# Kernel optimization log

Hardware: AMD Instinct MI355X
Metric: run time of the kernel (lower is better)

Reference implementation:

```python
import jax, jax.numpy as jnp
import numpy as np

#   per angular channel l: out_l = (1/sqrt(2l+1)) * sum_m x_nu[n,m,q] * x_1[n,m,p]
#   stacked over l with zero padding in the m axis (pad beyond 2l+1 is zero,
#   so the m-sum is unaffected), features flattened as full (q, p) outer product.

L = 4       # l = 0..3
N = 50000   # atomic environments (samples)
M = 7       # 2*l_max + 1
F_NU = 32   # features of density_nu per l
F_1 = 16    # features of density_1 per l


def setup_inputs() -> dict:
    key = jax.random.key(0)
    k1, k2 = jax.random.split(key)
    x_nu = jax.random.normal(k1, (L, N, M, F_NU), dtype=jnp.float32)
    x_1 = jax.random.normal(k2, (L, N, M, F_1), dtype=jnp.float32)
    ls = jnp.arange(L)
    # mask m-components beyond 2l+1 for each l  -> [L, M]
    mmask = (jnp.arange(M)[None, :] < (2 * ls + 1)[:, None]).astype(jnp.float32)
    x_nu = x_nu * mmask[:, None, :, None]
    x_1 = x_1 * mmask[:, None, :, None]
    return {"x_nu": x_nu, "x_1": x_1}


def reference(x_nu, x_1):
    # x_nu: [L, N, M, F_nu], x_1: [L, N, M, F_1]
    l_dim, n, _, f_nu = x_nu.shape
    f_1 = x_1.shape[-1]
    cg = 1.0 / jnp.sqrt(2.0 * jnp.arange(l_dim, dtype=jnp.float32) + 1.0)  # [L]
    # full (q_nu, q_1) outer product with sum over m, per l
    out = jnp.einsum('lnmq,lnmp->nlqp', x_nu, x_1)  # [N, L, F_nu, F_1]
    out = out * cg[None, :, None, None]
    return out.reshape(n, l_dim * f_nu * f_1)  # [N, L*F_nu*F_1]
```

## Files before the change

### kernel.cpp

```cpp
#include <hip/hip_runtime.h>


constexpr int L_DIM  = 4;
constexpr int M_DIM  = 7;
constexpr int FNU    = 32;
constexpr int F1     = 16;
constexpr int XNU_W  = L_DIM * M_DIM * FNU;
constexpr int X1_W   = L_DIM * M_DIM * F1;
constexpr int SAMP_W = XNU_W + X1_W;
constexpr int OUT_W  = L_DIM * FNU * F1;
constexpr int SPB    = 4;
constexpr int NV4    = SPB * SAMP_W / 4;
constexpr int NCHUNK = NV4 / 64;

typedef float f32x4 __attribute__((ext_vector_type(4)));

__global__ __launch_bounds__(256) void ps_kernel(
    const float* __restrict__ x_nu,
    const float* __restrict__ x_1,
    float* __restrict__ out,
    int N)
{
    __shared__ float lds[SPB * SAMP_W];
    const int t    = threadIdx.x;
    const int n0   = blockIdx.x * SPB;
    const int lane = t & 63;
    const int wid  = t >> 6;

    const float4* __restrict__ xnu4 = reinterpret_cast<const float4*>(x_nu);
    const float4* __restrict__ x14  = reinterpret_cast<const float4*>(x_1);
    float4* lds4 = reinterpret_cast<float4*>(lds);

    #pragma unroll
    for (int j = 0; j < 6; ++j) {
        const int c = wid + 4 * j;
        if (c < NCHUNK) {
            const int i = c * 64 + lane;
            int s = i / 336;
            int r = i - s * 336;
            int n = n0 + s;
            if (n >= N) n = N - 1;
            const float4* src;
            if (r < 224) {
                int l = r / 56, off = r - l * 56;
                src = &xnu4[(size_t)(l * N + n) * 56 + off];
            } else {
                int r2 = r - 224;
                int l = r2 / 28, off = r2 - l * 28;
                src = &x14[(size_t)(l * N + n) * 28 + off];
            }
            __builtin_amdgcn_global_load_lds(
                (const __attribute__((address_space(1))) void*)src,
                (__attribute__((address_space(3))) void*)&lds4[i],
                16, 0, 0);
        }
    }
    __syncthreads();

    const int u7 = t & 127;
    const int l  = u7 >> 5;
    const int u  = u7 & 31;
    const int pb = (u & 3) * 4;
    const int q2 = u >> 2;
    const float scale = rsqrtf(2.0f * (float)l + 1.0f);

    #pragma unroll
    for (int ss = 0; ss < 2; ++ss) {
        const int s = (t >> 7) + 2 * ss;
        const int n = n0 + s;
        if (n < N) {
            const float* xnu_s = lds + s * SAMP_W + l * (M_DIM * FNU);
            const float* x1_s  = lds + s * SAMP_W + XNU_W + l * (M_DIM * F1);

            float acc[4][4];
            #pragma unroll
            for (int k = 0; k < 4; ++k)
                #pragma unroll
                for (int j = 0; j < 4; ++j) acc[k][j] = 0.0f;

            #pragma unroll
            for (int m = 0; m < M_DIM; ++m) {
                float4 b = *reinterpret_cast<const float4*>(&x1_s[m * F1 + pb]);
                float a[4];
                #pragma unroll
                for (int k = 0; k < 4; ++k) a[k] = xnu_s[m * FNU + q2 + 8 * k];
                #pragma unroll
                for (int k = 0; k < 4; ++k) {
                    acc[k][0] += a[k] * b.x;
                    acc[k][1] += a[k] * b.y;
                    acc[k][2] += a[k] * b.z;
                    acc[k][3] += a[k] * b.w;
                }
            }

            float* outp = out + (size_t)n * OUT_W + l * (FNU * F1);
            #pragma unroll
            for (int k = 0; k < 4; ++k) {
                int q = q2 + 8 * k;
                f32x4 v = { acc[k][0] * scale, acc[k][1] * scale,
                            acc[k][2] * scale, acc[k][3] * scale };
                __builtin_nontemporal_store(v, reinterpret_cast<f32x4*>(&outp[q * F1 + pb]));
            }
        }
    }
}

extern "C" void kernel_launch(void* const* d_in, const int* in_sizes, int n_in,
                              void* d_out, int out_size, void* d_ws, size_t ws_size,
                              hipStream_t stream) {
    const float* x_nu = (const float*)d_in[0];
    const float* x_1  = (const float*)d_in[1];
    float* out = (float*)d_out;
    const int N = in_sizes[0] / XNU_W;
    const int blocks = (N + SPB - 1) / SPB;
    ps_kernel<<<blocks, 256, 0, stream>>>(x_nu, x_1, out, N);
}
```

Measured before the change: 580.8 us.

## Use persistent grid with double-buffered async LDS staging of sample groups

Replaces the one-block-per-group launch with a fixed grid of 512 persistent blocks. Each block loops over sample groups and prefetches the next group into a second LDS buffer with global_load_lds while computing the current one, using per-wave vmcnt waits and raw s_barrier. Output stores are switched from nontemporal to regular stores. The fixed grid may leave CUs underoccupied, and the hand-tuned vmcnt counts are fragile if the compiler issues a different number of loads.

```diff
diff --git a/kernel.cpp b/kernel.cpp
--- a/kernel.cpp
+++ b/kernel.cpp
@@ -10,10 +10,10 @@
 constexpr int SAMP_W = XNU_W + X1_W;
 constexpr int OUT_W  = L_DIM * FNU * F1;
 constexpr int SPB    = 4;
-constexpr int NV4    = SPB * SAMP_W / 4;
+constexpr int GRP_W  = SPB * SAMP_W;
+constexpr int NV4    = GRP_W / 4;
 constexpr int NCHUNK = NV4 / 64;
-
-typedef float f32x4 __attribute__((ext_vector_type(4)));
+constexpr int GRID   = 512;
 
 __global__ __launch_bounds__(256) void ps_kernel(
     const float* __restrict__ x_nu,
@@ -21,41 +21,42 @@
     float* __restrict__ out,
     int N)
 {
-    __shared__ float lds[SPB * SAMP_W];
+    __shared__ float lds[2 * GRP_W];
     const int t    = threadIdx.x;
-    const int n0   = blockIdx.x * SPB;
     const int lane = t & 63;
     const int wid  = t >> 6;
 
     const float4* __restrict__ xnu4 = reinterpret_cast<const float4*>(x_nu);
     const float4* __restrict__ x14  = reinterpret_cast<const float4*>(x_1);
-    float4* lds4 = reinterpret_cast<float4*>(lds);
 
-    #pragma unroll
-    for (int j = 0; j < 6; ++j) {
-        const int c = wid + 4 * j;
-        if (c < NCHUNK) {
-            const int i = c * 64 + lane;
-            int s = i / 336;
-            int r = i - s * 336;
-            int n = n0 + s;
-            if (n >= N) n = N - 1;
-            const float4* src;
-            if (r < 224) {
-                int l = r / 56, off = r - l * 56;
-                src = &xnu4[(size_t)(l * N + n) * 56 + off];
-            } else {
-                int r2 = r - 224;
-                int l = r2 / 28, off = r2 - l * 28;
-                src = &x14[(size_t)(l * N + n) * 28 + off];
+    auto stage = [&](int bufsel, int grp) {
+        const int gn0 = grp * SPB;
+        float4* dst4 = reinterpret_cast<float4*>(lds + bufsel * GRP_W);
+        #pragma unroll
+        for (int j = 0; j < 6; ++j) {
+            const int c = wid + 4 * j;
+            if (c < NCHUNK) {
+                const int i = c * 64 + lane;
+                int s = i / 336;
+                int r = i - s * 336;
+                int n = gn0 + s;
+                if (n >= N) n = N - 1;
+                const float4* src;
+                if (r < 224) {
+                    int l = r / 56, off = r - l * 56;
+                    src = &xnu4[(size_t)(l * N + n) * 56 + off];
+                } else {
+                    int r2 = r - 224;
+                    int l = r2 / 28, off = r2 - l * 28;
+                    src = &x14[(size_t)(l * N + n) * 28 + off];
+                }
+                __builtin_amdgcn_global_load_lds(
+                    (const __attribute__((address_space(1))) void*)src,
+                    (__attribute__((address_space(3))) void*)&dst4[i],
+                    16, 0, 0);
             }
-            __builtin_amdgcn_global_load_lds(
-                (const __attribute__((address_space(1))) void*)src,
-                (__attribute__((address_space(3))) void*)&lds4[i],
-                16, 0, 0);
         }
-    }
-    __syncthreads();
+    };
 
     const int u7 = t & 127;
     const int l  = u7 >> 5;
@@ -64,44 +65,64 @@
     const int q2 = u >> 2;
     const float scale = rsqrtf(2.0f * (float)l + 1.0f);
 
-    #pragma unroll
-    for (int ss = 0; ss < 2; ++ss) {
-        const int s = (t >> 7) + 2 * ss;
-        const int n = n0 + s;
-        if (n < N) {
-            const float* xnu_s = lds + s * SAMP_W + l * (M_DIM * FNU);
-            const float* x1_s  = lds + s * SAMP_W + XNU_W + l * (M_DIM * F1);
+    const int ngroups = (N + SPB - 1) / SPB;
+    const int stride  = gridDim.x;
 
-            float acc[4][4];
-            #pragma unroll
-            for (int k = 0; k < 4; ++k)
+    int g   = blockIdx.x;
+    int cur = 0;
+    stage(0, g);
+
+    for (; g < ngroups; g += stride) {
+        const int gn = g + stride;
+        if (gn < ngroups) stage(cur ^ 1, gn);
+
+        if (wid == 0) asm volatile("s_waitcnt vmcnt(6)" ::: "memory");
+        else          asm volatile("s_waitcnt vmcnt(5)" ::: "memory");
+        __builtin_amdgcn_s_barrier();
+        __builtin_amdgcn_sched_barrier(0);
+
+        #pragma unroll
+        for (int ss = 0; ss < 2; ++ss) {
+            const int s = (t >> 7) + 2 * ss;
+            const int n = g * SPB + s;
+            if (n < N) {
+                const float* xnu_s = lds + cur * GRP_W + s * SAMP_W + l * (M_DIM * FNU);
+                const float* x1_s  = lds + cur * GRP_W + s * SAMP_W + XNU_W + l * (M_DIM * F1);
+
+                float acc[4][4];
                 #pragma unroll
-                for (int j = 0; j < 4; ++j) acc[k][j] = 0.0f;
+                for (int k = 0; k < 4; ++k)
+                    #pragma unroll
+                    for (int j = 0; j < 4; ++j) acc[k][j] = 0.0f;
 
-            #pragma unroll
-            for (int m = 0; m < M_DIM; ++m) {
-                float4 b = *reinterpret_cast<const float4*>(&x1_s[m * F1 + pb]);
-                float a[4];
                 #pragma unroll
-                for (int k = 0; k < 4; ++k) a[k] = xnu_s[m * FNU + q2 + 8 * k];
+                for (int m = 0; m < M_DIM; ++m) {
+                    float4 b = *reinterpret_cast<const float4*>(&x1_s[m * F1 + pb]);
+                    float a[4];
+                    #pragma unroll
+                    for (int k = 0; k < 4; ++k) a[k] = xnu_s[m * FNU + q2 + 8 * k];
+                    #pragma unroll
+                    for (int k = 0; k < 4; ++k) {
+                        acc[k][0] += a[k] * b.x;
+                        acc[k][1] += a[k] * b.y;
+                        acc[k][2] += a[k] * b.z;
+                        acc[k][3] += a[k] * b.w;
+                    }
+                }
+
+                float* outp = out + (size_t)n * OUT_W + l * (FNU * F1);
                 #pragma unroll
                 for (int k = 0; k < 4; ++k) {
-                    acc[k][0] += a[k] * b.x;
-                    acc[k][1] += a[k] * b.y;
-                    acc[k][2] += a[k] * b.z;
-                    acc[k][3] += a[k] * b.w;
+                    int q = q2 + 8 * k;
+                    float4 v = make_float4(acc[k][0] * scale, acc[k][1] * scale,
+                                           acc[k][2] * scale, acc[k][3] * scale);
+                    *reinterpret_cast<float4*>(&outp[q * F1 + pb]) = v;
                 }
             }
+        }
 
-            float* outp = out + (size_t)n * OUT_W + l * (FNU * F1);
-            #pragma unroll
-            for (int k = 0; k < 4; ++k) {
-                int q = q2 + 8 * k;
-                f32x4 v = { acc[k][0] * scale, acc[k][1] * scale,
-                            acc[k][2] * scale, acc[k][3] * scale };
-                __builtin_nontemporal_store(v, reinterpret_cast<f32x4*>(&outp[q * F1 + pb]));
-            }
-        }
+        __builtin_amdgcn_s_barrier();
+        cur ^= 1;
     }
 }
 
@@ -112,6 +133,5 @@
     const float* x_1  = (const float*)d_in[1];
     float* out = (float*)d_out;
     const int N = in_sizes[0] / XNU_W;
-    const int blocks = (N + SPB - 1) / SPB;
-    ps_kernel<<<blocks, 256, 0, stream>>>(x_nu, x_1, out, N);
+    ps_kernel<<<GRID, 256, 0, stream>>>(x_nu, x_1, out, N);
 }
```

Measured after the change: 575.7 us. Within noise of the previous version (-0.9%).
